# Optimization experiments

Measured on AMD Instinct MI355X. Metric: run time of the kernel, lower is better.

The kernel has to match this reference:

```python
import jax, jax.numpy as jnp
import numpy as np

D = 1024      # model dim (used for theta exponent and 1/sqrt(d) scale)
D_H = 128     # head dim


def make_theta():
    # theta[i] = 10 ** (-2*(i-1)/d), each value repeated twice -> length d_H
    i = np.repeat(np.arange(D_H // 2), 2)
    return jnp.asarray(10.0 ** (-2.0 * (i - 1) / D), dtype=jnp.float32)


def rotation(x, theta):
    # x: [B, T, d_H]; positions are 1..T (source uses arange(1, T+1))
    B, T, dh = x.shape
    idx = jnp.arange(1, T + 1, dtype=x.dtype)[:, None]          # [T, 1]
    ang = idx * theta[None, :]                                   # [T, d_H]
    cos, sin = jnp.cos(ang), jnp.sin(ang)
    # pairwise swap with sign: (x0, x1) -> (x1, -x0)
    x2 = x.reshape(B, T, dh // 2, 2)
    swapped = jnp.stack([x2[..., 1], -x2[..., 0]], axis=-1).reshape(B, T, dh)
    return x * cos + swapped * sin


def setup_inputs() -> dict:
    key = jax.random.key(0)
    kx, kq, kk, kv = jax.random.split(key, 4)
    B, T = 4, 2048
    scale = 1.0 / np.sqrt(D)
    return {
        "x": jax.random.normal(kx, (B, T, D), dtype=jnp.float32),
        "Wq": jax.random.normal(kq, (D_H, D), dtype=jnp.float32) * scale,
        "Wk": jax.random.normal(kk, (D_H, D), dtype=jnp.float32) * scale,
        "Wv": jax.random.normal(kv, (D_H, D), dtype=jnp.float32) * scale,
        "theta": make_theta(),
    }


def reference(x, Wq, Wk, Wv, theta):
    B, T, d = x.shape
    Q = jnp.einsum('btd,hd->bth', x, Wq)
    K = jnp.einsum('btd,hd->bth', x, Wk)
    V = jnp.einsum('btd,hd->bth', x, Wv)
    Q = rotation(Q, theta)
    K = rotation(K, theta)
    # scale uses model dim d (not d_H), as in the source
    scores = jnp.einsum('bqh,bkh->bqk', Q, K) * (d ** -0.5)
    causal = jnp.tril(jnp.ones((T, T), dtype=bool))
    scores = jnp.where(causal, scores, -jnp.inf)
    attn = jax.nn.softmax(scores, axis=-1)
    return jnp.einsum('bqk,bkh->bqh', attn, V)
```

## Files before the change

kernel.cpp:

```cpp
#include <hip/hip_runtime.h>
#include <math.h>

#define T_SEQ 2048
#define D_MODEL 1024
#define DH 128
#define SLOTS 288
#define FRAG_B 262144

typedef __bf16 bfx8 __attribute__((ext_vector_type(8)));
typedef float f32x4 __attribute__((ext_vector_type(4)));

union U16x8 { uint4 u4; unsigned int ui[4]; unsigned short us[8]; __bf16 bf[8]; bfx8 v; };

__device__ inline uint4 cvt8u(float4 a, float4 b) {
    U16x8 u;
    u.bf[0] = (__bf16)a.x; u.bf[1] = (__bf16)a.y; u.bf[2] = (__bf16)a.z; u.bf[3] = (__bf16)a.w;
    u.bf[4] = (__bf16)b.x; u.bf[5] = (__bf16)b.y; u.bf[6] = (__bf16)b.z; u.bf[7] = (__bf16)b.w;
    return u.u4;
}

__device__ inline int slot_base32(int qt) {
    int g = qt >> 3, j = qt & 7;
    return 4 * g * (g + 1) + j * (g + 1);
}

__global__ __launch_bounds__(256) void prep_kernel(
    const float* __restrict__ x,
    const float* __restrict__ Wq, const float* __restrict__ Wk,
    const float* __restrict__ Wv,
    __bf16* __restrict__ xF, __bf16* __restrict__ WF, int nxb)
{
    const int bi = blockIdx.x;
    const int tid = threadIdx.x;

    if (bi < nxb) {
        __shared__ __align__(16) unsigned short Xs[64 * 72];
        const int m0 = (bi >> 4) * 64;
        const int k0 = (bi & 15) * 64;
        const int row = tid >> 2, cs = (tid & 3) * 16;
        const float* xp = x + (size_t)(m0 + row) * D_MODEL + k0 + cs;
        float4 a0 = *(const float4*)xp;
        float4 a1 = *(const float4*)(xp + 4);
        float4 a2 = *(const float4*)(xp + 8);
        float4 a3 = *(const float4*)(xp + 12);
        *(uint4*)&Xs[row * 72 + cs]     = cvt8u(a0, a1);
        *(uint4*)&Xs[row * 72 + cs + 8] = cvt8u(a2, a3);
        __syncthreads();
        const int L = tid & 63;
        #pragma unroll
        for (int rr = 0; rr < 2; ++rr) {
            const int fid = rr * 4 + (tid >> 6);
            const int mtl = fid >> 1, kcl = fid & 1;
            uint4 d = *(const uint4*)&Xs[(mtl * 16 + (L & 15)) * 72 + kcl * 32 + (L >> 4) * 8];
            const size_t frag = (size_t)((m0 >> 4) + mtl) * 32 + (k0 >> 5) + kcl;
            *(uint4*)&xF[frag * 512 + L * 8] = d;
        }
    } else {
        const int i = (bi - nxb) * 256 + tid;
        const int wsel = i >> 14;
        const int i2 = i & 16383;
        const int kc = i2 >> 9, j = (i2 >> 6) & 7, ln = i2 & 63;
        const int lo = ln & 15, quad = ln >> 4;
        const float* src = (wsel == 0) ? Wq : (wsel == 1) ? Wk : Wv;
        const float* p = src + (size_t)(j * 16 + lo) * D_MODEL + kc * 32 + quad * 8;
        float4 a = *(const float4*)p;
        float4 b = *(const float4*)(p + 4);
        *(uint4*)&WF[(size_t)((wsel * 32 + kc) * 8 + j) * 512 + ln * 8] = cvt8u(a, b);
    }
}

__global__ __launch_bounds__(64) void qkv_kernel(
    const __bf16* __restrict__ xF, const __bf16* __restrict__ WF,
    const float* __restrict__ theta,
    __bf16* __restrict__ QF, __bf16* __restrict__ KF, __bf16* __restrict__ VF)
{
    __shared__ __align__(16) unsigned short T[32 * 136];

    const int bx = blockIdx.x;
    const int wsel = bx >> 8;
    const int m0 = (bx & 255) * 32;

    const int ln = threadIdx.x;
    const int lo = ln & 15, quad = ln >> 4;

    const __bf16* WFp = WF + (size_t)wsel * (32 * 8 * 512);
    const size_t xf0 = ((size_t)(m0 >> 4)) * 32;

    bfx8 xc[2], xn[2], wc[8], wn[8];
    #pragma unroll
    for (int iq = 0; iq < 2; ++iq)
        xc[iq] = *(const bfx8*)&xF[(xf0 + iq * 32) * 512 + ln * 8];
    #pragma unroll
    for (int j = 0; j < 8; ++j)
        wc[j] = *(const bfx8*)&WFp[(size_t)j * 512 + ln * 8];

    f32x4 acc[2][8];
    #pragma unroll
    for (int iq = 0; iq < 2; ++iq)
        #pragma unroll
        for (int j = 0; j < 8; ++j) acc[iq][j] = (f32x4)(0.f);

    for (int kc = 0; kc < 32; ++kc) {
        if (kc < 31) {
            #pragma unroll
            for (int iq = 0; iq < 2; ++iq)
                xn[iq] = *(const bfx8*)&xF[(xf0 + iq * 32 + kc + 1) * 512 + ln * 8];
            #pragma unroll
            for (int j = 0; j < 8; ++j)
                wn[j] = *(const bfx8*)&WFp[(size_t)((kc + 1) * 8 + j) * 512 + ln * 8];
        }
        #pragma unroll
        for (int j = 0; j < 8; ++j) {
            acc[0][j] = __builtin_amdgcn_mfma_f32_16x16x32_bf16(xc[0], wc[j], acc[0][j], 0, 0, 0);
            acc[1][j] = __builtin_amdgcn_mfma_f32_16x16x32_bf16(xc[1], wc[j], acc[1][j], 0, 0, 0);
        }
        if (kc < 31) {
            xc[0] = xn[0]; xc[1] = xn[1];
            #pragma unroll
            for (int j = 0; j < 8; ++j) wc[j] = wn[j];
        }
    }

    const int b = m0 >> 11;
    const int mloc0 = m0 & (T_SEQ - 1);

    if (wsel < 2) {
        __bf16* dstP = (wsel == 0 ? QF : KF) + (size_t)b * FRAG_B;
        const int t16l = mloc0 >> 4;
        #pragma unroll
        for (int iq = 0; iq < 2; ++iq) {
            #pragma unroll
            for (int j = 0; j < 8; ++j) {
                const int h = j * 16 + lo;
                const float th = theta[h];
                #pragma unroll
                for (int r = 0; r < 4; ++r) {
                    const int pos = mloc0 + iq * 16 + quad * 4 + r + 1;
                    float v = acc[iq][j][r];
                    float partner = __shfl_xor(v, 1, 64);
                    float ang = (float)pos * th;
                    float rev = ang * 0.15915494309189535f;
                    rev -= floorf(rev);
                    float sn = __builtin_amdgcn_sinf(rev);
                    float cs = __builtin_amdgcn_cosf(rev);
                    float res = (h & 1) ? (v * cs - partner * sn)
                                        : (v * cs + partner * sn);
                    U16x8 u; u.bf[0] = (__bf16)res;
                    T[(quad * 4 + r) * 136 + h] = u.us[0];
                }
            }
            #pragma unroll
            for (int c4 = 0; c4 < 4; ++c4) {
                uint4 d = *(const uint4*)&T[(ln & 15) * 136 + c4 * 32 + (ln >> 4) * 8];
                *(uint4*)&dstP[(size_t)((t16l + iq) * 4 + c4) * 512 + ln * 8] = d;
            }
        }
    } else {
        const int kt32 = mloc0 >> 5;
        #pragma unroll
        for (int iq = 0; iq < 2; ++iq)
            #pragma unroll
            for (int j = 0; j < 8; ++j)
                #pragma unroll
                for (int r = 0; r < 4; ++r) {
                    U16x8 u; u.bf[0] = (__bf16)acc[iq][j][r];
                    T[(iq * 16 + quad * 4 + r) * 136 + j * 16 + lo] = u.us[0];
                }
        __bf16* dstP = VF + (size_t)b * FRAG_B;
        #pragma unroll
        for (int j = 0; j < 8; ++j) {
            U16x8 u;
            #pragma unroll
            for (int e = 0; e < 8; ++e)
                u.us[e] = T[((ln >> 4) * 8 + e) * 136 + j * 16 + (ln & 15)];
            *(uint4*)&dstP[(size_t)(kt32 * 8 + j) * 512 + ln * 8] = u.u4;
        }
    }
}

__global__ __launch_bounds__(64) void attn_partial_kernel(
    const __bf16* __restrict__ QF, const __bf16* __restrict__ KF,
    const __bf16* __restrict__ VF,
    __bf16* __restrict__ Opb, float* __restrict__ Ll)
{
    const int qt = blockIdx.x, c = blockIdx.y, b = blockIdx.z;
    const int qbase = qt * 32;
    const int kstart = c << 8;
    if (kstart > qbase) return;
    const int nt = min(8, (qbase + 32 - kstart) >> 5);

    __shared__ __align__(16) unsigned short Pw[2 * 640];

    const int ln = threadIdx.x;
    const int lo = ln & 15, quad = ln >> 4;
    const int hi8 = quad * 8;

    const __bf16* QFb = QF + (size_t)b * FRAG_B;
    const __bf16* KFb = KF + (size_t)b * FRAG_B;
    const __bf16* VFb = VF + (size_t)b * FRAG_B;

    bfx8 qf[2][4];
    #pragma unroll
    for (int iq = 0; iq < 2; ++iq)
        #pragma unroll
        for (int c4 = 0; c4 < 4; ++c4)
            qf[iq][c4] = *(const bfx8*)&QFb[(size_t)((qt * 2 + iq) * 4 + c4) * 512 + ln * 8];

    f32x4 O[2][8];
    #pragma unroll
    for (int iq = 0; iq < 2; ++iq)
        #pragma unroll
        for (int j = 0; j < 8; ++j) O[iq][j] = (f32x4)(0.f);
    float lsum[2][4];
    #pragma unroll
    for (int iq = 0; iq < 2; ++iq)
        #pragma unroll
        for (int r = 0; r < 4; ++r) lsum[iq][r] = 0.f;

    bfx8 kcur[2][4], knxt[2][4];
    #pragma unroll
    for (int jj = 0; jj < 2; ++jj)
        #pragma unroll
        for (int c4 = 0; c4 < 4; ++c4)
            kcur[jj][c4] = *(const bfx8*)&KFb[(size_t)(((kstart >> 4) + jj) * 4 + c4) * 512 + ln * 8];

    for (int kt = 0; kt < nt; ++kt) {
        const int k0 = kstart + kt * 32;
        bfx8 vf[8];
        #pragma unroll
        for (int j = 0; j < 8; ++j)
            vf[j] = *(const bfx8*)&VFb[(size_t)((k0 >> 5) * 8 + j) * 512 + ln * 8];
        if (kt + 1 < nt) {
            const int kn16 = (k0 + 32) >> 4;
            #pragma unroll
            for (int jj = 0; jj < 2; ++jj)
                #pragma unroll
                for (int c4 = 0; c4 < 4; ++c4)
                    knxt[jj][c4] = *(const bfx8*)&KFb[(size_t)((kn16 + jj) * 4 + c4) * 512 + ln * 8];
        }

        f32x4 s4[2][2];
        #pragma unroll
        for (int iq = 0; iq < 2; ++iq)
            #pragma unroll
            for (int jj = 0; jj < 2; ++jj) s4[iq][jj] = (f32x4)(0.f);
        #pragma unroll
        for (int c4 = 0; c4 < 4; ++c4)
            #pragma unroll
            for (int iq = 0; iq < 2; ++iq)
                #pragma unroll
                for (int jj = 0; jj < 2; ++jj)
                    s4[iq][jj] = __builtin_amdgcn_mfma_f32_16x16x32_bf16(qf[iq][c4], kcur[jj][c4], s4[iq][jj], 0, 0, 0);

        const bool needMask = (k0 + 31 > qbase);
        #pragma unroll
        for (int iq = 0; iq < 2; ++iq)
            #pragma unroll
            for (int jj = 0; jj < 2; ++jj)
                #pragma unroll
                for (int r = 0; r < 4; ++r) {
                    const int col = k0 + jj * 16 + lo;
                    const int row = qbase + iq * 16 + quad * 4 + r;
                    float p = __expf(s4[iq][jj][r] * 0.03125f);
                    if (needMask && col > row) p = 0.f;
                    lsum[iq][r] += p;
                    U16x8 u; u.bf[0] = (__bf16)p;
                    Pw[iq * 640 + (quad * 4 + r) * 40 + jj * 16 + lo] = u.us[0];
                }

        bfx8 pf0 = *(const bfx8*)&Pw[lo * 40 + hi8];
        bfx8 pf1 = *(const bfx8*)&Pw[640 + lo * 40 + hi8];
        #pragma unroll
        for (int j = 0; j < 8; ++j) {
            O[0][j] = __builtin_amdgcn_mfma_f32_16x16x32_bf16(pf0, vf[j], O[0][j], 0, 0, 0);
            O[1][j] = __builtin_amdgcn_mfma_f32_16x16x32_bf16(pf1, vf[j], O[1][j], 0, 0, 0);
        }

        #pragma unroll
        for (int jj = 0; jj < 2; ++jj)
            #pragma unroll
            for (int c4 = 0; c4 < 4; ++c4) kcur[jj][c4] = knxt[jj][c4];
    }

    #pragma unroll
    for (int off = 1; off < 16; off <<= 1)
        #pragma unroll
        for (int iq = 0; iq < 2; ++iq)
            #pragma unroll
            for (int r = 0; r < 4; ++r) lsum[iq][r] += __shfl_xor(lsum[iq][r], off, 64);

    const size_t sb = (size_t)b * SLOTS + slot_base32(qt) + c;
    #pragma unroll
    for (int iq = 0; iq < 2; ++iq)
        #pragma unroll
        for (int j = 0; j < 8; ++j) {
            U16x8 u;
            u.bf[0] = (__bf16)O[iq][j][0]; u.bf[1] = (__bf16)O[iq][j][1];
            u.bf[2] = (__bf16)O[iq][j][2]; u.bf[3] = (__bf16)O[iq][j][3];
            *(uint2*)&Opb[((sb * 2 + iq) * 8 + j) * 256 + ln * 4] = make_uint2(u.ui[0], u.ui[1]);
        }
    if (lo == 0) {
        #pragma unroll
        for (int iq = 0; iq < 2; ++iq)
            #pragma unroll
            for (int r = 0; r < 4; ++r)
                Ll[sb * 32 + iq * 16 + quad * 4 + r] = lsum[iq][r];
    }
}

__global__ __launch_bounds__(128) void attn_merge_kernel(
    const __bf16* __restrict__ Opb, const float* __restrict__ Ll,
    float* __restrict__ out)
{
    const int qt = blockIdx.x, b = blockIdx.y, j = blockIdx.z;
    const int g = qt >> 3, nc = g + 1;
    const size_t base = (size_t)b * SLOTS + slot_base32(qt);

    __shared__ float Lsh[8][32];
    const int tid = threadIdx.x;
    const int iq = tid >> 6, ln = tid & 63;
    const int lo = ln & 15, quad = ln >> 4;

    for (int idx = tid; idx < nc * 32; idx += 128)
        Lsh[idx >> 5][idx & 31] = Ll[(base + (idx >> 5)) * 32 + (idx & 31)];
    __syncthreads();

    float acc[4] = {0.f, 0.f, 0.f, 0.f};
    for (int cc = 0; cc < nc; ++cc) {
        uint2 d = *(const uint2*)&Opb[(((base + cc) * 2 + iq) * 8 + j) * 256 + ln * 4];
        U16x8 u; u.ui[0] = d.x; u.ui[1] = d.y;
        #pragma unroll
        for (int r = 0; r < 4; ++r) acc[r] += (float)u.bf[r];
    }

    #pragma unroll
    for (int r = 0; r < 4; ++r) {
        const int row = iq * 16 + quad * 4 + r;
        float l = 0.f;
        for (int cc = 0; cc < nc; ++cc) l += Lsh[cc][row];
        out[((size_t)b * T_SEQ + qt * 32 + row) * DH + j * 16 + lo] = acc[r] / l;
    }
}

extern "C" void kernel_launch(void* const* d_in, const int* in_sizes, int n_in,
                              void* d_out, int out_size, void* d_ws, size_t ws_size,
                              hipStream_t stream) {
    const float* x     = (const float*)d_in[0];
    const float* Wq    = (const float*)d_in[1];
    const float* Wk    = (const float*)d_in[2];
    const float* Wv    = (const float*)d_in[3];
    const float* theta = (const float*)d_in[4];
    float* out = (float*)d_out;

    const int M = in_sizes[0] / D_MODEL;
    const int B = M / T_SEQ;

    __bf16* xF  = (__bf16*)d_ws;
    __bf16* WF  = xF + (size_t)M * D_MODEL;
    __bf16* QF  = WF + (size_t)3 * 32 * 8 * 512;
    __bf16* KF  = QF + (size_t)B * FRAG_B;
    __bf16* VF  = KF + (size_t)B * FRAG_B;
    __bf16* Opb = VF + (size_t)B * FRAG_B;
    float*  Ll  = (float*)(Opb + (size_t)B * SLOTS * 2 * 8 * 256);

    const int nxb = (M / 64) * 16;
    prep_kernel<<<dim3(nxb + 192), 256, 0, stream>>>(x, Wq, Wk, Wv, xF, WF, nxb);
    qkv_kernel<<<dim3(3 * (M / 32)), 64, 0, stream>>>(xF, WF, theta, QF, KF, VF);
    attn_partial_kernel<<<dim3(T_SEQ / 32, 8, B), 64, 0, stream>>>(QF, KF, VF, Opb, Ll);
    attn_merge_kernel<<<dim3(T_SEQ / 32, B, 8), 128, 0, stream>>>(Opb, Ll, out);
}
```

Measured before the change: 126.1 us.

## Fuse x bf16 conversion into QKV GEMM, reading fp32 x directly

```diff
diff --git a/kernel.cpp b/kernel.cpp
--- a/kernel.cpp
+++ b/kernel.cpp
@@ -19,58 +19,36 @@
     return u.u4;
 }
 
+__device__ inline bfx8 cvt8v(float4 a, float4 b) {
+    U16x8 u;
+    u.bf[0] = (__bf16)a.x; u.bf[1] = (__bf16)a.y; u.bf[2] = (__bf16)a.z; u.bf[3] = (__bf16)a.w;
+    u.bf[4] = (__bf16)b.x; u.bf[5] = (__bf16)b.y; u.bf[6] = (__bf16)b.z; u.bf[7] = (__bf16)b.w;
+    return u.v;
+}
+
 __device__ inline int slot_base32(int qt) {
     int g = qt >> 3, j = qt & 7;
     return 4 * g * (g + 1) + j * (g + 1);
 }
 
-__global__ __launch_bounds__(256) void prep_kernel(
-    const float* __restrict__ x,
+__global__ __launch_bounds__(256) void prep_w_kernel(
     const float* __restrict__ Wq, const float* __restrict__ Wk,
-    const float* __restrict__ Wv,
-    __bf16* __restrict__ xF, __bf16* __restrict__ WF, int nxb)
+    const float* __restrict__ Wv, __bf16* __restrict__ WF)
 {
-    const int bi = blockIdx.x;
-    const int tid = threadIdx.x;
-
-    if (bi < nxb) {
-        __shared__ __align__(16) unsigned short Xs[64 * 72];
-        const int m0 = (bi >> 4) * 64;
-        const int k0 = (bi & 15) * 64;
-        const int row = tid >> 2, cs = (tid & 3) * 16;
-        const float* xp = x + (size_t)(m0 + row) * D_MODEL + k0 + cs;
-        float4 a0 = *(const float4*)xp;
-        float4 a1 = *(const float4*)(xp + 4);
-        float4 a2 = *(const float4*)(xp + 8);
-        float4 a3 = *(const float4*)(xp + 12);
-        *(uint4*)&Xs[row * 72 + cs]     = cvt8u(a0, a1);
-        *(uint4*)&Xs[row * 72 + cs + 8] = cvt8u(a2, a3);
-        __syncthreads();
-        const int L = tid & 63;
-        #pragma unroll
-        for (int rr = 0; rr < 2; ++rr) {
-            const int fid = rr * 4 + (tid >> 6);
-            const int mtl = fid >> 1, kcl = fid & 1;
-            uint4 d = *(const uint4*)&Xs[(mtl * 16 + (L & 15)) * 72 + kcl * 32 + (L >> 4) * 8];
-            const size_t frag = (size_t)((m0 >> 4) + mtl) * 32 + (k0 >> 5) + kcl;
-            *(uint4*)&xF[frag * 512 + L * 8] = d;
-        }
-    } else {
-        const int i = (bi - nxb) * 256 + tid;
-        const int wsel = i >> 14;
-        const int i2 = i & 16383;
-        const int kc = i2 >> 9, j = (i2 >> 6) & 7, ln = i2 & 63;
-        const int lo = ln & 15, quad = ln >> 4;
-        const float* src = (wsel == 0) ? Wq : (wsel == 1) ? Wk : Wv;
-        const float* p = src + (size_t)(j * 16 + lo) * D_MODEL + kc * 32 + quad * 8;
-        float4 a = *(const float4*)p;
-        float4 b = *(const float4*)(p + 4);
-        *(uint4*)&WF[(size_t)((wsel * 32 + kc) * 8 + j) * 512 + ln * 8] = cvt8u(a, b);
-    }
+    const int i = blockIdx.x * 256 + threadIdx.x;
+    const int wsel = i >> 14;
+    const int i2 = i & 16383;
+    const int kc = i2 >> 9, j = (i2 >> 6) & 7, ln = i2 & 63;
+    const int lo = ln & 15, quad = ln >> 4;
+    const float* src = (wsel == 0) ? Wq : (wsel == 1) ? Wk : Wv;
+    const float* p = src + (size_t)(j * 16 + lo) * D_MODEL + kc * 32 + quad * 8;
+    float4 a = *(const float4*)p;
+    float4 b = *(const float4*)(p + 4);
+    *(uint4*)&WF[(size_t)((wsel * 32 + kc) * 8 + j) * 512 + ln * 8] = cvt8u(a, b);
 }
 
 __global__ __launch_bounds__(64) void qkv_kernel(
-    const __bf16* __restrict__ xF, const __bf16* __restrict__ WF,
+    const float* __restrict__ x, const __bf16* __restrict__ WF,
     const float* __restrict__ theta,
     __bf16* __restrict__ QF, __bf16* __restrict__ KF, __bf16* __restrict__ VF)
 {
@@ -84,15 +62,21 @@
     const int lo = ln & 15, quad = ln >> 4;
 
     const __bf16* WFp = WF + (size_t)wsel * (32 * 8 * 512);
-    const size_t xf0 = ((size_t)(m0 >> 4)) * 32;
-
-    bfx8 xc[2], xn[2], wc[8], wn[8];
-    #pragma unroll
-    for (int iq = 0; iq < 2; ++iq)
-        xc[iq] = *(const bfx8*)&xF[(xf0 + iq * 32) * 512 + ln * 8];
-    #pragma unroll
-    for (int j = 0; j < 8; ++j)
-        wc[j] = *(const bfx8*)&WFp[(size_t)j * 512 + ln * 8];
+    const float* xr0 = x + (size_t)(m0 + lo) * D_MODEL + quad * 8;
+    const float* xr1 = xr0 + (size_t)16 * D_MODEL;
+
+    float4 xA[2][2], xB[2][2];
+    bfx8 wA[8], wB[8];
+
+    xA[0][0] = *(const float4*)(xr0);      xA[0][1] = *(const float4*)(xr0 + 4);
+    xA[1][0] = *(const float4*)(xr1);      xA[1][1] = *(const float4*)(xr1 + 4);
+    xB[0][0] = *(const float4*)(xr0 + 32); xB[0][1] = *(const float4*)(xr0 + 36);
+    xB[1][0] = *(const float4*)(xr1 + 32); xB[1][1] = *(const float4*)(xr1 + 36);
+    #pragma unroll
+    for (int j = 0; j < 8; ++j) {
+        wA[j] = *(const bfx8*)&WFp[(size_t)j * 512 + ln * 8];
+        wB[j] = *(const bfx8*)&WFp[(size_t)(8 + j) * 512 + ln * 8];
+    }
 
     f32x4 acc[2][8];
     #pragma unroll
@@ -100,24 +84,36 @@
         #pragma unroll
         for (int j = 0; j < 8; ++j) acc[iq][j] = (f32x4)(0.f);
 
-    for (int kc = 0; kc < 32; ++kc) {
-        if (kc < 31) {
-            #pragma unroll
-            for (int iq = 0; iq < 2; ++iq)
-                xn[iq] = *(const bfx8*)&xF[(xf0 + iq * 32 + kc + 1) * 512 + ln * 8];
-            #pragma unroll
-            for (int j = 0; j < 8; ++j)
-                wn[j] = *(const bfx8*)&WFp[(size_t)((kc + 1) * 8 + j) * 512 + ln * 8];
-        }
-        #pragma unroll
-        for (int j = 0; j < 8; ++j) {
-            acc[0][j] = __builtin_amdgcn_mfma_f32_16x16x32_bf16(xc[0], wc[j], acc[0][j], 0, 0, 0);
-            acc[1][j] = __builtin_amdgcn_mfma_f32_16x16x32_bf16(xc[1], wc[j], acc[1][j], 0, 0, 0);
-        }
-        if (kc < 31) {
-            xc[0] = xn[0]; xc[1] = xn[1];
-            #pragma unroll
-            for (int j = 0; j < 8; ++j) wc[j] = wn[j];
+    for (int kc = 0; kc < 32; kc += 2) {
+        {
+            const int kp = (kc + 2 < 32) ? (kc + 2) : kc;
+            bfx8 x0 = cvt8v(xA[0][0], xA[0][1]);
+            bfx8 x1 = cvt8v(xA[1][0], xA[1][1]);
+            xA[0][0] = *(const float4*)(xr0 + kp * 32);
+            xA[0][1] = *(const float4*)(xr0 + kp * 32 + 4);
+            xA[1][0] = *(const float4*)(xr1 + kp * 32);
+            xA[1][1] = *(const float4*)(xr1 + kp * 32 + 4);
+            #pragma unroll
+            for (int j = 0; j < 8; ++j) {
+                acc[0][j] = __builtin_amdgcn_mfma_f32_16x16x32_bf16(x0, wA[j], acc[0][j], 0, 0, 0);
+                acc[1][j] = __builtin_amdgcn_mfma_f32_16x16x32_bf16(x1, wA[j], acc[1][j], 0, 0, 0);
+                wA[j] = *(const bfx8*)&WFp[(size_t)(kp * 8 + j) * 512 + ln * 8];
+            }
+        }
+        {
+            const int kp = (kc + 3 < 32) ? (kc + 3) : (kc + 1);
+            bfx8 x0 = cvt8v(xB[0][0], xB[0][1]);
+            bfx8 x1 = cvt8v(xB[1][0], xB[1][1]);
+            xB[0][0] = *(const float4*)(xr0 + kp * 32);
+            xB[0][1] = *(const float4*)(xr0 + kp * 32 + 4);
+            xB[1][0] = *(const float4*)(xr1 + kp * 32);
+            xB[1][1] = *(const float4*)(xr1 + kp * 32 + 4);
+            #pragma unroll
+            for (int j = 0; j < 8; ++j) {
+                acc[0][j] = __builtin_amdgcn_mfma_f32_16x16x32_bf16(x0, wB[j], acc[0][j], 0, 0, 0);
+                acc[1][j] = __builtin_amdgcn_mfma_f32_16x16x32_bf16(x1, wB[j], acc[1][j], 0, 0, 0);
+                wB[j] = *(const bfx8*)&WFp[(size_t)(kp * 8 + j) * 512 + ln * 8];
+            }
         }
     }
 
@@ -355,17 +351,15 @@
     const int M = in_sizes[0] / D_MODEL;
     const int B = M / T_SEQ;
 
-    __bf16* xF  = (__bf16*)d_ws;
-    __bf16* WF  = xF + (size_t)M * D_MODEL;
+    __bf16* WF  = (__bf16*)d_ws;
     __bf16* QF  = WF + (size_t)3 * 32 * 8 * 512;
     __bf16* KF  = QF + (size_t)B * FRAG_B;
     __bf16* VF  = KF + (size_t)B * FRAG_B;
     __bf16* Opb = VF + (size_t)B * FRAG_B;
     float*  Ll  = (float*)(Opb + (size_t)B * SLOTS * 2 * 8 * 256);
 
-    const int nxb = (M / 64) * 16;
-    prep_kernel<<<dim3(nxb + 192), 256, 0, stream>>>(x, Wq, Wk, Wv, xF, WF, nxb);
-    qkv_kernel<<<dim3(3 * (M / 32)), 64, 0, stream>>>(xF, WF, theta, QF, KF, VF);
+    prep_w_kernel<<<dim3(192), 256, 0, stream>>>(Wq, Wk, Wv, WF);
+    qkv_kernel<<<dim3(3 * (M / 32)), 64, 0, stream>>>(x, WF, theta, QF, KF, VF);
     attn_partial_kernel<<<dim3(T_SEQ / 32, 8, B), 64, 0, stream>>>(QF, KF, VF, Opb, Ll);
     attn_merge_kernel<<<dim3(T_SEQ / 32, B, 8), 128, 0, stream>>>(Opb, Ll, out);
 }
```

Measured after the change: 143.0 us. 1.13x slower.

## Split QKV projection into smaller per-wave tiles for more parallelism

Applied to the files above, without the earlier changes.

```diff
diff --git a/kernel.cpp b/kernel.cpp
--- a/kernel.cpp
+++ b/kernel.cpp
@@ -77,98 +77,145 @@
     __shared__ __align__(16) unsigned short T[32 * 136];
 
     const int bx = blockIdx.x;
-    const int wsel = bx >> 8;
-    const int m0 = (bx & 255) * 32;
-
     const int ln = threadIdx.x;
     const int lo = ln & 15, quad = ln >> 4;
 
-    const __bf16* WFp = WF + (size_t)wsel * (32 * 8 * 512);
-    const size_t xf0 = ((size_t)(m0 >> 4)) * 32;
-
-    bfx8 xc[2], xn[2], wc[8], wn[8];
-    #pragma unroll
-    for (int iq = 0; iq < 2; ++iq)
-        xc[iq] = *(const bfx8*)&xF[(xf0 + iq * 32) * 512 + ln * 8];
-    #pragma unroll
-    for (int j = 0; j < 8; ++j)
-        wc[j] = *(const bfx8*)&WFp[(size_t)j * 512 + ln * 8];
-
-    f32x4 acc[2][8];
-    #pragma unroll
-    for (int iq = 0; iq < 2; ++iq)
-        #pragma unroll
-        for (int j = 0; j < 8; ++j) acc[iq][j] = (f32x4)(0.f);
-
-    for (int kc = 0; kc < 32; ++kc) {
-        if (kc < 31) {
-            #pragma unroll
-            for (int iq = 0; iq < 2; ++iq)
-                xn[iq] = *(const bfx8*)&xF[(xf0 + iq * 32 + kc + 1) * 512 + ln * 8];
-            #pragma unroll
-            for (int j = 0; j < 8; ++j)
-                wn[j] = *(const bfx8*)&WFp[(size_t)((kc + 1) * 8 + j) * 512 + ln * 8];
-        }
-        #pragma unroll
-        for (int j = 0; j < 8; ++j) {
-            acc[0][j] = __builtin_amdgcn_mfma_f32_16x16x32_bf16(xc[0], wc[j], acc[0][j], 0, 0, 0);
-            acc[1][j] = __builtin_amdgcn_mfma_f32_16x16x32_bf16(xc[1], wc[j], acc[1][j], 0, 0, 0);
-        }
-        if (kc < 31) {
-            xc[0] = xn[0]; xc[1] = xn[1];
-            #pragma unroll
-            for (int j = 0; j < 8; ++j) wc[j] = wn[j];
-        }
-    }
-
-    const int b = m0 >> 11;
-    const int mloc0 = m0 & (T_SEQ - 1);
-
-    if (wsel < 2) {
-        __bf16* dstP = (wsel == 0 ? QF : KF) + (size_t)b * FRAG_B;
-        const int t16l = mloc0 >> 4;
-        #pragma unroll
-        for (int iq = 0; iq < 2; ++iq) {
-            #pragma unroll
-            for (int j = 0; j < 8; ++j) {
-                const int h = j * 16 + lo;
-                const float th = theta[h];
+    if (bx < 2048) {
+        const int wsel01 = bx >> 10;
+        const int sub = (bx >> 8) & 3;
+        const int iq = sub >> 1, jh = sub & 1;
+        const int mt = bx & 255;
+        const int mt16 = mt * 2 + iq;
+
+        const __bf16* WFp = WF + (size_t)wsel01 * (32 * 8 * 512) + (size_t)jh * (4 * 512);
+        const size_t xb = (size_t)mt16 * 32;
+
+        bfx8 xA = *(const bfx8*)&xF[(xb + 0) * 512 + ln * 8];
+        bfx8 xB = *(const bfx8*)&xF[(xb + 1) * 512 + ln * 8];
+        bfx8 wA[4], wB[4];
+        #pragma unroll
+        for (int jl = 0; jl < 4; ++jl) {
+            wA[jl] = *(const bfx8*)&WFp[(size_t)jl * 512 + ln * 8];
+            wB[jl] = *(const bfx8*)&WFp[(size_t)(8 + jl) * 512 + ln * 8];
+        }
+
+        f32x4 acc[4];
+        #pragma unroll
+        for (int jl = 0; jl < 4; ++jl) acc[jl] = (f32x4)(0.f);
+
+        for (int kc = 0; kc < 32; kc += 2) {
+            const int kpA = (kc + 2 < 32) ? kc + 2 : kc;
+            #pragma unroll
+            for (int jl = 0; jl < 4; ++jl) {
+                acc[jl] = __builtin_amdgcn_mfma_f32_16x16x32_bf16(xA, wA[jl], acc[jl], 0, 0, 0);
+                wA[jl] = *(const bfx8*)&WFp[((size_t)kpA * 8 + jl) * 512 + ln * 8];
+            }
+            xA = *(const bfx8*)&xF[(xb + kpA) * 512 + ln * 8];
+            const int kpB = (kc + 3 < 32) ? kc + 3 : kc + 1;
+            #pragma unroll
+            for (int jl = 0; jl < 4; ++jl) {
+                acc[jl] = __builtin_amdgcn_mfma_f32_16x16x32_bf16(xB, wB[jl], acc[jl], 0, 0, 0);
+                wB[jl] = *(const bfx8*)&WFp[((size_t)kpB * 8 + jl) * 512 + ln * 8];
+            }
+            xB = *(const bfx8*)&xF[(xb + kpB) * 512 + ln * 8];
+        }
+
+        const int b = mt16 >> 7;
+        const int t16 = mt16 & 127;
+        const int mloc16 = t16 * 16;
+        __bf16* dstP = (wsel01 == 0 ? QF : KF) + (size_t)b * FRAG_B;
+
+        #pragma unroll
+        for (int jl = 0; jl < 4; ++jl) {
+            const int j = jh * 4 + jl;
+            const int h = j * 16 + lo;
+            const float th = theta[h];
+            #pragma unroll
+            for (int r = 0; r < 4; ++r) {
+                const int pos = mloc16 + quad * 4 + r + 1;
+                float v = acc[jl][r];
+                float partner = __shfl_xor(v, 1, 64);
+                float ang = (float)pos * th;
+                float rev = ang * 0.15915494309189535f;
+                rev -= floorf(rev);
+                float sn = __builtin_amdgcn_sinf(rev);
+                float cs = __builtin_amdgcn_cosf(rev);
+                float res = (h & 1) ? (v * cs - partner * sn)
+                                    : (v * cs + partner * sn);
+                U16x8 u; u.bf[0] = (__bf16)res;
+                T[(quad * 4 + r) * 136 + h] = u.us[0];
+            }
+        }
+        #pragma unroll
+        for (int c4l = 0; c4l < 2; ++c4l) {
+            const int c4 = jh * 2 + c4l;
+            uint4 d = *(const uint4*)&T[(ln & 15) * 136 + c4 * 32 + (ln >> 4) * 8];
+            *(uint4*)&dstP[(size_t)(t16 * 4 + c4) * 512 + ln * 8] = d;
+        }
+    } else {
+        const int r2 = bx - 2048;
+        const int jh = r2 >> 8;
+        const int mt = r2 & 255;
+        const int mt16 = mt * 2;
+
+        const __bf16* WFp = WF + (size_t)2 * (32 * 8 * 512) + (size_t)jh * (4 * 512);
+        const size_t xb0 = (size_t)mt16 * 32, xb1 = xb0 + 32;
+
+        bfx8 xA[2], xB[2], wA[4], wB[4];
+        xA[0] = *(const bfx8*)&xF[(xb0 + 0) * 512 + ln * 8];
+        xA[1] = *(const bfx8*)&xF[(xb1 + 0) * 512 + ln * 8];
+        xB[0] = *(const bfx8*)&xF[(xb0 + 1) * 512 + ln * 8];
+        xB[1] = *(const bfx8*)&xF[(xb1 + 1) * 512 + ln * 8];
+        #pragma unroll
+        for (int jl = 0; jl < 4; ++jl) {
+            wA[jl] = *(const bfx8*)&WFp[(size_t)jl * 512 + ln * 8];
+            wB[jl] = *(const bfx8*)&WFp[(size_t)(8 + jl) * 512 + ln * 8];
+        }
+
+        f32x4 acc[2][4];
+        #pragma unroll
+        for (int iq = 0; iq < 2; ++iq)
+            #pragma unroll
+            for (int jl = 0; jl < 4; ++jl) acc[iq][jl] = (f32x4)(0.f);
+
+        for (int kc = 0; kc < 32; kc += 2) {
+            const int kpA = (kc + 2 < 32) ? kc + 2 : kc;
+            #pragma unroll
+            for (int jl = 0; jl < 4; ++jl) {
+                acc[0][jl] = __builtin_amdgcn_mfma_f32_16x16x32_bf16(xA[0], wA[jl], acc[0][jl], 0, 0, 0);
+                acc[1][jl] = __builtin_amdgcn_mfma_f32_16x16x32_bf16(xA[1], wA[jl], acc[1][jl], 0, 0, 0);
+                wA[jl] = *(const bfx8*)&WFp[((size_t)kpA * 8 + jl) * 512 + ln * 8];
+            }
+            xA[0] = *(const bfx8*)&xF[(xb0 + kpA) * 512 + ln * 8];
+            xA[1] = *(const bfx8*)&xF[(xb1 + kpA) * 512 + ln * 8];
+            const int kpB = (kc + 3 < 32) ? kc + 3 : kc + 1;
+            #pragma unroll
+            for (int jl = 0; jl < 4; ++jl) {
+                acc[0][jl] = __builtin_amdgcn_mfma_f32_16x16x32_bf16(xB[0], wB[jl], acc[0][jl], 0, 0, 0);
+                acc[1][jl] = __builtin_amdgcn_mfma_f32_16x16x32_bf16(xB[1], wB[jl], acc[1][jl], 0, 0, 0);
+                wB[jl] = *(const bfx8*)&WFp[((size_t)kpB * 8 + jl) * 512 + ln * 8];
+            }
+            xB[0] = *(const bfx8*)&xF[(xb0 + kpB) * 512 + ln * 8];
+            xB[1] = *(const bfx8*)&xF[(xb1 + kpB) * 512 + ln * 8];
+        }
+
+        const int b = mt >> 6;
+        const int kt32 = mt & 63;
+        #pragma unroll
+        for (int iq = 0; iq < 2; ++iq)
+            #pragma unroll
+            for (int jl = 0; jl < 4; ++jl) {
+                const int j = jh * 4 + jl;
                 #pragma unroll
                 for (int r = 0; r < 4; ++r) {
-                    const int pos = mloc0 + iq * 16 + quad * 4 + r + 1;
-                    float v = acc[iq][j][r];
-                    float partner = __shfl_xor(v, 1, 64);
-                    float ang = (float)pos * th;
-                    float rev = ang * 0.15915494309189535f;
-                    rev -= floorf(rev);
-                    float sn = __builtin_amdgcn_sinf(rev);
-                    float cs = __builtin_amdgcn_cosf(rev);
-                    float res = (h & 1) ? (v * cs - partner * sn)
-                                        : (v * cs + partner * sn);
-                    U16x8 u; u.bf[0] = (__bf16)res;
-                    T[(quad * 4 + r) * 136 + h] = u.us[0];
-                }
-            }
-            #pragma unroll
-            for (int c4 = 0; c4 < 4; ++c4) {
-                uint4 d = *(const uint4*)&T[(ln & 15) * 136 + c4 * 32 + (ln >> 4) * 8];
-                *(uint4*)&dstP[(size_t)((t16l + iq) * 4 + c4) * 512 + ln * 8] = d;
-            }
-        }
-    } else {
-        const int kt32 = mloc0 >> 5;
-        #pragma unroll
-        for (int iq = 0; iq < 2; ++iq)
-            #pragma unroll
-            for (int j = 0; j < 8; ++j)
-                #pragma unroll
-                for (int r = 0; r < 4; ++r) {
-                    U16x8 u; u.bf[0] = (__bf16)acc[iq][j][r];
+                    U16x8 u; u.bf[0] = (__bf16)acc[iq][jl][r];
                     T[(iq * 16 + quad * 4 + r) * 136 + j * 16 + lo] = u.us[0];
                 }
+            }
         __bf16* dstP = VF + (size_t)b * FRAG_B;
         #pragma unroll
-        for (int j = 0; j < 8; ++j) {
+        for (int jl = 0; jl < 4; ++jl) {
+            const int j = jh * 4 + jl;
             U16x8 u;
             #pragma unroll
             for (int e = 0; e < 8; ++e)
@@ -365,7 +412,7 @@
 
     const int nxb = (M / 64) * 16;
     prep_kernel<<<dim3(nxb + 192), 256, 0, stream>>>(x, Wq, Wk, Wv, xF, WF, nxb);
-    qkv_kernel<<<dim3(3 * (M / 32)), 64, 0, stream>>>(xF, WF, theta, QF, KF, VF);
+    qkv_kernel<<<dim3(2048 + 512), 64, 0, stream>>>(xF, WF, theta, QF, KF, VF);
     attn_partial_kernel<<<dim3(T_SEQ / 32, 8, B), 64, 0, stream>>>(QF, KF, VF, Opb, Ll);
     attn_merge_kernel<<<dim3(T_SEQ / 32, B, 8), 128, 0, stream>>>(Opb, Ll, out);
 }
```

New measurement: 123.7 us. About the same (-2.0%).
